# Kernel optimization log

Measured on AMD Instinct MI355X. Metric: run time of the kernel, lower is better.

The kernel has to match this reference:

```python
import jax, jax.numpy as jnp
import numpy as np

HEADS = 4

def _topk_mask(attn, k):
    # exact replica of mask.scatter_(-1, topk_indices, 1.0): exactly k ones per row
    C = attn.shape[-1]
    _, idx = jax.lax.top_k(attn, k)                      # [b,h,C,k]
    return jax.nn.one_hot(idx, C, dtype=attn.dtype).sum(axis=-2) > 0  # [b,h,C,C] bool


def setup_inputs() -> dict:
    key = jax.random.key(0)
    ks = jax.random.split(key, 8)
    b, dim, h, w = 32, 128, 4096, 1
    s = 0.05
    return {
        "x": jax.random.normal(ks[0], (b, dim, h, w), jnp.float32),
        "qkv_w": jax.random.normal(ks[1], (3 * dim, dim), jnp.float32) * s,
        "qkv_b": jax.random.normal(ks[2], (3 * dim,), jnp.float32) * s,
        "dw_w": jax.random.normal(ks[3], (3 * dim, 1, 3, 3), jnp.float32) * s,
        "dw_b": jax.random.normal(ks[4], (3 * dim,), jnp.float32) * s,
        "proj_w": jax.random.normal(ks[5], (dim, dim), jnp.float32) * s,
        "proj_b": jax.random.normal(ks[6], (dim,), jnp.float32) * s,
        "temperature": jnp.ones((HEADS, 1, 1), jnp.float32),
        "attn_w": jnp.full((4,), 0.2, jnp.float32),  # attn1..attn4
    }


def reference(x, qkv_w, qkv_b, dw_w, dw_b, proj_w, proj_b, temperature, attn_w):
    b, c, h, w = x.shape
    # 1x1 conv qkv, then 3x3 depthwise conv (groups = 3*c)
    qkv = jnp.einsum('bchw,oc->bohw', x, qkv_w) + qkv_b[None, :, None, None]
    qkv = jax.lax.conv_general_dilated(
        qkv, dw_w, window_strides=(1, 1), padding=((1, 1), (1, 1)),
        dimension_numbers=('NCHW', 'OIHW', 'NCHW'), feature_group_count=3 * c
    ) + dw_b[None, :, None, None]
    q, k, v = jnp.split(qkv, 3, axis=1)
    heads = lambda t: t.reshape(b, HEADS, c // HEADS, h * w)  # b head c (hw)
    q, k, v = heads(q), heads(k), heads(v)
    # F.normalize(dim=-1), eps=1e-12
    q = q / jnp.maximum(jnp.linalg.norm(q, axis=-1, keepdims=True), 1e-12)
    k = k / jnp.maximum(jnp.linalg.norm(k, axis=-1, keepdims=True), 1e-12)
    C = c // HEADS
    attn = jnp.einsum('bhcn,bhdn->bhcd', q, k) * temperature[None]  # [b,head,C,C]
    top_ks = [C // 2, (2 * C) // 3, (3 * C) // 4, (4 * C) // 5]
    out = jnp.zeros_like(v)
    for i, kk in enumerate(top_ks):
        m = _topk_mask(attn, kk)
        a = jax.nn.softmax(jnp.where(m, attn, -jnp.inf), axis=-1)
        out = out + attn_w[i] * jnp.einsum('bhcd,bhdn->bhcn', a, v)
    out = out.reshape(b, c, h, w)
    out = jnp.einsum('bchw,oc->bohw', out, proj_w) + proj_b[None, :, None, None]
    return out
```

## Files before the change

kernel.cpp:

```cpp
#include <hip/hip_runtime.h>

#define B_ 32
#define CD 128
#define O3 384
#define N  4096
#define H_ 4
#define C_ 32

typedef __bf16 bf16x8 __attribute__((ext_vector_type(8)));
typedef float floatx4 __attribute__((ext_vector_type(4)));

#define MFMA16(a, b, c) __builtin_amdgcn_mfma_f32_16x16x32_bf16(a, b, c, 0, 0, 0)

__device__ __forceinline__ float b2f(unsigned int u) {
  return __builtin_bit_cast(float, u << 16);
}
__device__ __forceinline__ float b2fh(unsigned int u) {
  return __builtin_bit_cast(float, u & 0xffff0000u);
}
__device__ __forceinline__ unsigned short f2b(float f) {
  unsigned int bits = __builtin_bit_cast(unsigned int, f);
  unsigned int r = (bits + 0x7FFFu + ((bits >> 16) & 1u)) >> 16;
  return (unsigned short)r;
}

__global__ __launch_bounds__(256) void k0_xt(const float* __restrict__ x,
                                             unsigned short* __restrict__ xT)
{
  __shared__ float xt[32 * 68];
  const int t = threadIdx.x;
  const int n0 = blockIdx.x * 64, c0 = blockIdx.y * 32, b = blockIdx.z;
  const float* xb = x + ((size_t)b * CD + c0) * N + n0;
#pragma unroll
  for (int i = 0; i < 2; i++) {
    int f = i * 256 + t;
    int c = f >> 4, n4 = (f & 15) * 4;
    float4 v = *(const float4*)(xb + (size_t)c * N + n4);
    *(float4*)&xt[c * 68 + n4] = v;
  }
  __syncthreads();
  int n = t >> 2, cb = (t & 3) * 8;
  unsigned short tmp[8];
#pragma unroll
  for (int j = 0; j < 8; j++) tmp[j] = f2b(xt[(cb + j) * 68 + n]);
  *(uint4*)(xT + ((size_t)b * N + n0 + n) * CD + c0 + cb) = *(uint4*)tmp;
}

__global__ void k0_w(const float* __restrict__ qkv_w,
                     const float* __restrict__ proj_w,
                     unsigned short* __restrict__ qkv_wb,
                     unsigned short* __restrict__ proj_wb)
{
  int e = (blockIdx.x * 256 + threadIdx.x) * 4;
  const float* src; unsigned short* dst; int off;
  if (e < 49152) { src = qkv_w; dst = qkv_wb; off = e; }
  else           { src = proj_w; dst = proj_wb; off = e - 49152; }
  float4 v = *(const float4*)(src + off);
  unsigned short tmp[4] = {f2b(v.x), f2b(v.y), f2b(v.z), f2b(v.w)};
  *(uint2*)(dst + off) = *(uint2*)tmp;
}

__global__ __launch_bounds__(256, 4) void k1_qkv_dw(
    const unsigned short* __restrict__ xT, const unsigned short* __restrict__ qkv_wb,
    const float* __restrict__ qkv_b, const float* __restrict__ dw_w,
    const float* __restrict__ dw_b, unsigned short* __restrict__ qkvd,
    unsigned short* __restrict__ vT)
{
  __shared__ __align__(16) char smem[34816];
  unsigned short* Bs   = (unsigned short*)smem;
  unsigned short* pres = (unsigned short*)smem;

  const int t = threadIdx.x;
  const int ytile = blockIdx.x, otile = blockIdx.y, b = blockIdx.z;
  const int obase = otile * 128;
  const int ybase = ytile * 124;
  const int wv = t >> 6, l = t & 63, quad = l >> 4, lm = l & 15;

#pragma unroll
  for (int i = 0; i < 8; i++) {
    int f = i * 256 + t;
    int row = f >> 4, c8 = (f & 15) * 8;
    int yg = ybase - 2 + row;
    uint4 v = make_uint4(0u, 0u, 0u, 0u);
    if (yg >= 0 && yg < N)
      v = *(const uint4*)(xT + ((size_t)b * N + yg) * CD + c8);
    *(uint4*)&Bs[row * 136 + c8] = v;
  }
  __syncthreads();

  floatx4 acc[2][8];
#pragma unroll
  for (int mt = 0; mt < 2; mt++)
#pragma unroll
    for (int nt = 0; nt < 8; nt++) acc[mt][nt] = (floatx4){0.f, 0.f, 0.f, 0.f};

  const unsigned short* wbase =
      qkv_wb + (size_t)(obase + wv * 32 + lm) * CD + quad * 8;
#pragma unroll
  for (int ks = 0; ks < 4; ks++) {
    bf16x8 a0 = *(const bf16x8*)(wbase + ks * 32);
    bf16x8 a1 = *(const bf16x8*)(wbase + 16 * CD + ks * 32);
#pragma unroll
    for (int nt = 0; nt < 8; nt++) {
      bf16x8 bb = *(const bf16x8*)&Bs[(nt * 16 + lm) * 136 + ks * 32 + quad * 8];
      acc[0][nt] = MFMA16(a0, bb, acc[0][nt]);
      acc[1][nt] = MFMA16(a1, bb, acc[1][nt]);
    }
  }

  if (otile < 2) {
    __syncthreads();
#pragma unroll
    for (int mt = 0; mt < 2; mt++)
#pragma unroll
      for (int r = 0; r < 4; r++) {
        int o = wv * 32 + mt * 16 + quad * 4 + r;
        float bias = qkv_b[obase + o];
#pragma unroll
        for (int nt = 0; nt < 8; nt++) {
          int i = nt * 16 + lm;
          if (i >= 1) {
            int yg = ybase - 2 + i;
            pres[o * 132 + (i - 1)] =
                f2b((yg >= 0 && yg < N) ? (acc[mt][nt][r] + bias) : 0.f);
          }
        }
      }
    __syncthreads();
    const int p = t & 63, og = t >> 6;
    const bool ok = (p < 62) && (ybase + 2 * p < N);
    const unsigned int* presu = (const unsigned int*)pres;
    for (int r2 = 0; r2 < 32; r2++) {
      int oo = __builtin_amdgcn_readfirstlane(obase + og * 32 + r2);
      float w0 = dw_w[oo * 9 + 1], w1 = dw_w[oo * 9 + 4],
            w2 = dw_w[oo * 9 + 7], db = dw_b[oo];
      int o = oo - obase;
      unsigned int u0 = presu[(o * 132 >> 1) + p];
      unsigned int u1 = presu[(o * 132 >> 1) + p + 1];
      float v0 = b2f(u0), v1 = b2fh(u0), v2 = b2f(u1), v3 = b2fh(u1);
      float out0 = w0 * v0 + w1 * v1 + w2 * v2 + db;
      float out1 = w0 * v1 + w1 * v2 + w2 * v3 + db;
      unsigned int pk = (unsigned int)f2b(out0) |
                        ((unsigned int)f2b(out1) << 16);
      if (ok)
        *(unsigned int*)(qkvd + ((size_t)b * 256 + oo) * N + ybase + 2 * p) = pk;
    }
  } else {
    const int o = t & 127, half = t >> 7;
    const int oo = obase + o;
    const float w0 = dw_w[oo * 9 + 1], w1 = dw_w[oo * 9 + 4],
                w2 = dw_w[oo * 9 + 7], db = dw_b[oo];
    __syncthreads();
#pragma unroll
    for (int mt = 0; mt < 2; mt++)
#pragma unroll
      for (int r = 0; r < 4; r++) {
        int o2 = wv * 32 + mt * 16 + quad * 4 + r;
        float bias = qkv_b[obase + o2];
#pragma unroll
        for (int nt = 0; nt < 8; nt++) {
          int i = nt * 16 + lm;
          int yg = ybase - 2 + i;
          pres[i * 132 + o2] =
              f2b((yg >= 0 && yg < N) ? (acc[mt][nt][r] + bias) : 0.f);
        }
      }
    __syncthreads();
    int i0 = 2 + half * 62;
    float pm = b2f((unsigned int)pres[(i0 - 1) * 132 + o]);
    float pc = b2f((unsigned int)pres[i0 * 132 + o]);
    for (int i = i0; i < i0 + 62; i++) {
      float pp = b2f((unsigned int)pres[(i + 1) * 132 + o]);
      int yo = ybase - 2 + i;
      if (yo < N) {
        float v = w0 * pm + w1 * pc + w2 * pp + db;
        vT[((size_t)b * N + yo) * CD + o] = f2b(v);
      }
      pm = pc; pc = pp;
    }
  }
}

__global__ __launch_bounds__(256, 4) void k3_gram(
    const unsigned short* __restrict__ qkvd, float* __restrict__ part)
{
  __shared__ float red[4 * 8 * 272];
  const int ns = blockIdx.x, h = blockIdx.y, b = blockIdx.z;
  const int t = threadIdx.x;
  const int wv = t >> 6, l = t & 63, quad = l >> 4, lm = l & 15;
  const unsigned short* qb = qkvd + ((size_t)b * 256 + h * C_) * N;
  const unsigned short* kb = qkvd + ((size_t)b * 256 + 128 + h * C_) * N;

  floatx4 acc[8];
#pragma unroll
  for (int i = 0; i < 8; i++) acc[i] = (floatx4){0.f, 0.f, 0.f, 0.f};

  const int nbase = ns * 1024 + wv * 32 + quad * 8;
#pragma unroll
  for (int ch = 0; ch < 8; ch++) {
    int nc = nbase + ch * 128;
    bf16x8 a0 = *(const bf16x8*)(qb + (size_t)lm * N + nc);
    bf16x8 a1 = *(const bf16x8*)(qb + (size_t)(16 + lm) * N + nc);
    bf16x8 b0 = *(const bf16x8*)(kb + (size_t)lm * N + nc);
    bf16x8 b1 = *(const bf16x8*)(kb + (size_t)(16 + lm) * N + nc);
    acc[0] = MFMA16(a0, b0, acc[0]);
    acc[1] = MFMA16(a0, b1, acc[1]);
    acc[2] = MFMA16(a1, b0, acc[2]);
    acc[3] = MFMA16(a1, b1, acc[3]);
    acc[4] = MFMA16(a0, a0, acc[4]);
    acc[5] = MFMA16(a1, a1, acc[5]);
    acc[6] = MFMA16(b0, b0, acc[6]);
    acc[7] = MFMA16(b1, b1, acc[7]);
  }

#pragma unroll
  for (int tl = 0; tl < 8; tl++)
#pragma unroll
    for (int r = 0; r < 4; r++)
      red[wv * 2176 + tl * 272 + (quad * 4 + r) * 17 + lm] = acc[tl][r];
  __syncthreads();

  float* pb = part + ((size_t)(b * H_ + h) * 4 + ns) * 2048;
  for (int e = t; e < 2048; e += 256) {
    int tl = e >> 8, rc = e & 255, row = rc >> 4, col = rc & 15;
    int a = tl * 272 + row * 17 + col;
    float s = red[a] + red[2176 + a] + red[2 * 2176 + a] + red[3 * 2176 + a];
    if (tl < 4) {
      int mt = tl >> 1, nt = tl & 1;
      pb[(mt * 16 + row) * 32 + nt * 16 + col] = s;
    } else if (row == col) {
      if (tl < 6) pb[1024 + (tl - 4) * 16 + row] = s;
      else        pb[1056 + (tl - 6) * 16 + row] = s;
    }
  }
}

__global__ __launch_bounds__(256) void k45(
    const float* __restrict__ part, const unsigned short* __restrict__ proj_wb,
    const float* __restrict__ temperature, const float* __restrict__ attn_w,
    unsigned short* __restrict__ Mb)
{
  __shared__ float La[H_][C_][33];
  __shared__ float sq2[256];
  __shared__ float rn[256];
  __shared__ float exL[H_][C_][33];
  __shared__ unsigned char rkL[H_][C_][C_];
  __shared__ unsigned short AwtT[H_][C_][40];
  const int b = blockIdx.x, t = threadIdx.x;

  const float* pbb = part + (size_t)b * 32768;
  for (int e = t; e < 4 * 2048; e += 256) {
    int h = e >> 11, idx = e & 2047;
    if (idx < 1088) {
      const float* p = pbb + h * 8192 + idx;
      float s = p[0] + p[2048] + p[2 * 2048] + p[3 * 2048];
      if (idx < 1024) La[h][idx >> 5][idx & 31] = s;
      else if (idx < 1056) sq2[h * 32 + (idx - 1024)] = s;
      else sq2[128 + h * 32 + (idx - 1056)] = s;
    }
  }
  __syncthreads();
  rn[t] = 1.f / fmaxf(sqrtf(sq2[t]), 1e-12f);
  __syncthreads();
  for (int e = t; e < 4096; e += 256) {
    int h = e >> 10, i = (e >> 5) & 31, j = e & 31;
    La[h][i][j] *= rn[h * 32 + i] * rn[128 + h * 32 + j] * temperature[h];
  }
  __syncthreads();

  if (t < 128) {
    int h = t >> 5, i = t & 31;
    float m = -1e30f;
    for (int j = 0; j < 32; j++) m = fmaxf(m, La[h][i][j]);
    float S0 = 0.f, S1 = 0.f, S2 = 0.f, S3 = 0.f;
    for (int j = 0; j < 32; j++) {
      float vj = La[h][i][j];
      int r = 0;
      for (int j2 = 0; j2 < 32; j2++) {
        float v2 = La[h][i][j2];
        r += (v2 > vj) || (v2 == vj && j2 < j);
      }
      float e = __expf(vj - m);
      exL[h][i][j] = e;
      rkL[h][i][j] = (unsigned char)r;
      if (r < 16) S0 += e;
      if (r < 21) S1 += e;
      if (r < 24) S2 += e;
      if (r < 25) S3 += e;
    }
    float w0 = attn_w[0] / S0, w1 = attn_w[1] / S1;
    float w2 = attn_w[2] / S2, w3 = attn_w[3] / S3;
    for (int j = 0; j < 32; j++) {
      int r = rkL[h][i][j];
      float cmb = (r < 16 ? w0 : 0.f) + (r < 21 ? w1 : 0.f) +
                  (r < 24 ? w2 : 0.f) + (r < 25 ? w3 : 0.f);
      AwtT[h][j][i] = f2b(exL[h][i][j] * cmb);
    }
  }
  __syncthreads();

  {
    const int wv = t >> 6, l = t & 63, quad = l >> 4, lm = l & 15;
    const int h = wv;
    bf16x8 bfr[2];
#pragma unroll
    for (int jt = 0; jt < 2; jt++)
      bfr[jt] = *(const bf16x8*)&AwtT[h][jt * 16 + lm][quad * 8];
#pragma unroll
    for (int mt = 0; mt < 8; mt++) {
      bf16x8 a = *(const bf16x8*)(proj_wb +
                    (size_t)(mt * 16 + lm) * CD + h * C_ + quad * 8);
#pragma unroll
      for (int jt = 0; jt < 2; jt++) {
        floatx4 acc = (floatx4){0.f, 0.f, 0.f, 0.f};
        acc = MFMA16(a, bfr[jt], acc);
#pragma unroll
        for (int r = 0; r < 4; r++) {
          int row = quad * 4 + r;
          Mb[(size_t)b * 16384 + (mt * 16 + row) * CD + h * C_ + jt * 16 + lm] =
              f2b(acc[r]);
        }
      }
    }
  }
}

__global__ __launch_bounds__(256, 4) void k6_out(
    const unsigned short* __restrict__ vT, const unsigned short* __restrict__ Mb,
    const float* __restrict__ proj_b, float* __restrict__ out)
{
  __shared__ unsigned short Bs[128 * 136];
  const int t = threadIdx.x;
  const int y0 = blockIdx.x * 128, b = blockIdx.y;
  const int wv = t >> 6, l = t & 63, quad = l >> 4, lm = l & 15;

#pragma unroll
  for (int i = 0; i < 8; i++) {
    int f = i * 256 + t;
    int row = f >> 4, c8 = (f & 15) * 8;
    *(uint4*)&Bs[row * 136 + c8] =
        *(const uint4*)(vT + ((size_t)b * N + y0 + row) * CD + c8);
  }
  __syncthreads();

  floatx4 acc[2][8];
#pragma unroll
  for (int mt = 0; mt < 2; mt++)
#pragma unroll
    for (int nt = 0; nt < 8; nt++) acc[mt][nt] = (floatx4){0.f, 0.f, 0.f, 0.f};

  const unsigned short* mbase =
      Mb + (size_t)b * 16384 + (size_t)(wv * 32 + lm) * CD + quad * 8;
#pragma unroll
  for (int ks = 0; ks < 4; ks++) {
    bf16x8 a0 = *(const bf16x8*)(mbase + ks * 32);
    bf16x8 a1 = *(const bf16x8*)(mbase + 16 * CD + ks * 32);
#pragma unroll
    for (int nt = 0; nt < 8; nt++) {
      bf16x8 bb = *(const bf16x8*)&Bs[(nt * 16 + lm) * 136 + ks * 32 + quad * 8];
      acc[0][nt] = MFMA16(a0, bb, acc[0][nt]);
      acc[1][nt] = MFMA16(a1, bb, acc[1][nt]);
    }
  }

#pragma unroll
  for (int mt = 0; mt < 2; mt++)
#pragma unroll
    for (int r = 0; r < 4; r++) {
      int o = wv * 32 + mt * 16 + quad * 4 + r;
      float pb = proj_b[o];
#pragma unroll
      for (int nt = 0; nt < 8; nt++) {
        int y = y0 + nt * 16 + lm;
        out[((size_t)b * CD + o) * N + y] = acc[mt][nt][r] + pb;
      }
    }
}

extern "C" void kernel_launch(void* const* d_in, const int* in_sizes, int n_in,
                              void* d_out, int out_size, void* d_ws, size_t ws_size,
                              hipStream_t stream)
{
  (void)in_sizes; (void)n_in; (void)out_size; (void)ws_size;
  const float* x           = (const float*)d_in[0];
  const float* qkv_w       = (const float*)d_in[1];
  const float* qkv_b       = (const float*)d_in[2];
  const float* dw_w        = (const float*)d_in[3];
  const float* dw_b        = (const float*)d_in[4];
  const float* proj_w      = (const float*)d_in[5];
  const float* proj_b      = (const float*)d_in[6];
  const float* temperature = (const float*)d_in[7];
  const float* attn_w      = (const float*)d_in[8];
  float* out = (float*)d_out;

  unsigned short* xT      = (unsigned short*)d_ws;
  unsigned short* qkv_wb  = xT + (size_t)16777216;
  unsigned short* proj_wb = qkv_wb + 49152;
  unsigned short* qkvd    = proj_wb + 16384;
  unsigned short* vT      = qkvd + (size_t)33554432;
  unsigned short* Mb      = vT + (size_t)16777216;
  float* part = (float*)(Mb + 524288);

  k0_xt    <<<dim3(64, 4, 32),  256, 0, stream>>>(x, xT);
  k0_w     <<<dim3(64),         256, 0, stream>>>(qkv_w, proj_w, qkv_wb, proj_wb);
  k1_qkv_dw<<<dim3(34, 3, 32),  256, 0, stream>>>(xT, qkv_wb, qkv_b, dw_w, dw_b,
                                                  qkvd, vT);
  k3_gram  <<<dim3(4, H_, B_),  256, 0, stream>>>(qkvd, part);
  k45      <<<dim3(B_),         256, 0, stream>>>(part, proj_wb, temperature,
                                                  attn_w, Mb);
  k6_out   <<<dim3(32, B_),     256, 0, stream>>>(vT, Mb, proj_b, out);
}
```

Measured before the change: 268.9 us.

## Fold depthwise conv taps into qkv weights and compute as single K=384 GEMM

Since w=1, the 3x3 depthwise conv reduces to a 3-tap conv along h, which is linear after the 1x1 qkv conv. The change folds the tap weights into a 384-wide weight matrix so each block runs one GEMM over three shifted copies of the input, with bias and boundary corrections precomputed. This removes the LDS staging pass and the separate depthwise loop, and the swizzled LDS layout is meant to avoid bank conflicts. In exchange it triples the MFMA work in k1 and rounds the tap-scaled weights to bf16. Workspace buffers Mb and part are reused for the new weights and bias tables before the kernels that later write to them.

```diff
diff --git a/kernel.cpp b/kernel.cpp
--- a/kernel.cpp
+++ b/kernel.cpp
@@ -48,135 +48,154 @@
 
 __global__ void k0_w(const float* __restrict__ qkv_w,
                      const float* __restrict__ proj_w,
-                     unsigned short* __restrict__ qkv_wb,
-                     unsigned short* __restrict__ proj_wb)
-{
-  int e = (blockIdx.x * 256 + threadIdx.x) * 4;
-  const float* src; unsigned short* dst; int off;
-  if (e < 49152) { src = qkv_w; dst = qkv_wb; off = e; }
-  else           { src = proj_w; dst = proj_wb; off = e - 49152; }
-  float4 v = *(const float4*)(src + off);
-  unsigned short tmp[4] = {f2b(v.x), f2b(v.y), f2b(v.z), f2b(v.w)};
-  *(uint2*)(dst + off) = *(uint2*)tmp;
+                     const float* __restrict__ dw_w,
+                     const float* __restrict__ dw_b,
+                     const float* __restrict__ qkv_b,
+                     unsigned short* __restrict__ qkv_wb2,
+                     unsigned short* __restrict__ proj_wb,
+                     float* __restrict__ sb,
+                     float* __restrict__ c0,
+                     float* __restrict__ c2)
+{
+  int e = blockIdx.x * 256 + threadIdx.x;
+  if (e < 36864) {
+    int base = e * 4;
+    int o = base / 384;
+    int k = base - o * 384;
+    int dlt = k >> 7, c = k & 127;
+    float w = dw_w[o * 9 + 1 + 3 * dlt];
+    float4 q = *(const float4*)(qkv_w + o * 128 + c);
+    unsigned short tmp[4] = {f2b(w * q.x), f2b(w * q.y), f2b(w * q.z),
+                             f2b(w * q.w)};
+    *(uint2*)(qkv_wb2 + base) = *(uint2*)tmp;
+  } else if (e < 40960) {
+    int base = (e - 36864) * 4;
+    float4 v = *(const float4*)(proj_w + base);
+    unsigned short tmp[4] = {f2b(v.x), f2b(v.y), f2b(v.z), f2b(v.w)};
+    *(uint2*)(proj_wb + base) = *(uint2*)tmp;
+  } else if (e < 41344) {
+    int o = e - 40960;
+    float w0 = dw_w[o * 9 + 1], w1 = dw_w[o * 9 + 4], w2 = dw_w[o * 9 + 7];
+    float qb = qkv_b[o], db = dw_b[o];
+    sb[o] = qb * (w0 + w1 + w2) + db;
+    c0[o] = qb * w0;
+    c2[o] = qb * w2;
+  }
 }
 
 __global__ __launch_bounds__(256, 4) void k1_qkv_dw(
-    const unsigned short* __restrict__ xT, const unsigned short* __restrict__ qkv_wb,
-    const float* __restrict__ qkv_b, const float* __restrict__ dw_w,
-    const float* __restrict__ dw_b, unsigned short* __restrict__ qkvd,
+    const unsigned short* __restrict__ xT,
+    const unsigned short* __restrict__ qkv_wb2,
+    const float* __restrict__ sb, const float* __restrict__ c0,
+    const float* __restrict__ c2, unsigned short* __restrict__ qkvd,
     unsigned short* __restrict__ vT)
 {
-  __shared__ __align__(16) char smem[34816];
-  unsigned short* Bs   = (unsigned short*)smem;
-  unsigned short* pres = (unsigned short*)smem;
-
+  __shared__ unsigned short Bs[128 * 128];
   const int t = threadIdx.x;
   const int ytile = blockIdx.x, otile = blockIdx.y, b = blockIdx.z;
   const int obase = otile * 128;
-  const int ybase = ytile * 124;
+  const int ybase = ytile * 126;
   const int wv = t >> 6, l = t & 63, quad = l >> 4, lm = l & 15;
 
 #pragma unroll
   for (int i = 0; i < 8; i++) {
     int f = i * 256 + t;
-    int row = f >> 4, c8 = (f & 15) * 8;
-    int yg = ybase - 2 + row;
+    int row = f >> 4, ch = f & 15;
+    int yg = ybase - 1 + row;
     uint4 v = make_uint4(0u, 0u, 0u, 0u);
     if (yg >= 0 && yg < N)
-      v = *(const uint4*)(xT + ((size_t)b * N + yg) * CD + c8);
-    *(uint4*)&Bs[row * 136 + c8] = v;
-  }
-  __syncthreads();
-
-  floatx4 acc[2][8];
-#pragma unroll
-  for (int mt = 0; mt < 2; mt++)
-#pragma unroll
-    for (int nt = 0; nt < 8; nt++) acc[mt][nt] = (floatx4){0.f, 0.f, 0.f, 0.f};
+      v = *(const uint4*)(xT + ((size_t)b * N + yg) * CD + ch * 8);
+    *(uint4*)&Bs[row * 128 + ((ch ^ (row & 15)) << 3)] = v;
+  }
+  __syncthreads();
 
   const unsigned short* wbase =
-      qkv_wb + (size_t)(obase + wv * 32 + lm) * CD + quad * 8;
-#pragma unroll
-  for (int ks = 0; ks < 4; ks++) {
-    bf16x8 a0 = *(const bf16x8*)(wbase + ks * 32);
-    bf16x8 a1 = *(const bf16x8*)(wbase + 16 * CD + ks * 32);
-#pragma unroll
-    for (int nt = 0; nt < 8; nt++) {
-      bf16x8 bb = *(const bf16x8*)&Bs[(nt * 16 + lm) * 136 + ks * 32 + quad * 8];
-      acc[0][nt] = MFMA16(a0, bb, acc[0][nt]);
-      acc[1][nt] = MFMA16(a1, bb, acc[1][nt]);
-    }
-  }
+      qkv_wb2 + (size_t)(obase + wv * 32 + lm) * 384 + quad * 8;
+  const bool edge = (ybase == 0) || (ybase + 126 >= N);
 
   if (otile < 2) {
-    __syncthreads();
+    floatx4 acc[2][8];
 #pragma unroll
     for (int mt = 0; mt < 2; mt++)
 #pragma unroll
+      for (int nt = 0; nt < 8; nt++) acc[mt][nt] = (floatx4){0.f, 0.f, 0.f, 0.f};
+
+#pragma unroll
+    for (int ks = 0; ks < 12; ks++) {
+      bf16x8 a0 = *(const bf16x8*)(wbase + ks * 32);
+      bf16x8 a1 = *(const bf16x8*)(wbase + 16 * 384 + ks * 32);
+      const int dlt = ks >> 2, cpart = ks & 3;
+      const int swz = (((cpart << 2) + quad) ^ ((lm + dlt) & 15)) << 3;
+#pragma unroll
+      for (int nt = 0; nt < 8; nt++) {
+        int rr = nt * 16 + lm + dlt;
+        if (nt == 7) rr = (rr > 127) ? 127 : rr;
+        bf16x8 bb = *(const bf16x8*)&Bs[rr * 128 + swz];
+        acc[0][nt] = MFMA16(a0, bb, acc[0][nt]);
+        acc[1][nt] = MFMA16(a1, bb, acc[1][nt]);
+      }
+    }
+
+#pragma unroll
+    for (int mt = 0; mt < 2; mt++)
+#pragma unroll
       for (int r = 0; r < 4; r++) {
-        int o = wv * 32 + mt * 16 + quad * 4 + r;
-        float bias = qkv_b[obase + o];
+        const int o = obase + wv * 32 + mt * 16 + quad * 4 + r;
+        const float bias = sb[o];
+        float c0v = 0.f, c2v = 0.f;
+        if (edge) { c0v = c0[o]; c2v = c2[o]; }
+        const size_t orow = ((size_t)b * 256 + o) * N;
 #pragma unroll
         for (int nt = 0; nt < 8; nt++) {
-          int i = nt * 16 + lm;
-          if (i >= 1) {
-            int yg = ybase - 2 + i;
-            pres[o * 132 + (i - 1)] =
-                f2b((yg >= 0 && yg < N) ? (acc[mt][nt][r] + bias) : 0.f);
-          }
+          int iy = nt * 16 + lm;
+          int y = ybase + iy;
+          float val = acc[mt][nt][r] + bias;
+          if (y == 0) val -= c0v;
+          if (y == N - 1) val -= c2v;
+          if (iy < 126 && y < N) qkvd[orow + y] = f2b(val);
         }
       }
-    __syncthreads();
-    const int p = t & 63, og = t >> 6;
-    const bool ok = (p < 62) && (ybase + 2 * p < N);
-    const unsigned int* presu = (const unsigned int*)pres;
-    for (int r2 = 0; r2 < 32; r2++) {
-      int oo = __builtin_amdgcn_readfirstlane(obase + og * 32 + r2);
-      float w0 = dw_w[oo * 9 + 1], w1 = dw_w[oo * 9 + 4],
-            w2 = dw_w[oo * 9 + 7], db = dw_b[oo];
-      int o = oo - obase;
-      unsigned int u0 = presu[(o * 132 >> 1) + p];
-      unsigned int u1 = presu[(o * 132 >> 1) + p + 1];
-      float v0 = b2f(u0), v1 = b2fh(u0), v2 = b2f(u1), v3 = b2fh(u1);
-      float out0 = w0 * v0 + w1 * v1 + w2 * v2 + db;
-      float out1 = w0 * v1 + w1 * v2 + w2 * v3 + db;
-      unsigned int pk = (unsigned int)f2b(out0) |
-                        ((unsigned int)f2b(out1) << 16);
-      if (ok)
-        *(unsigned int*)(qkvd + ((size_t)b * 256 + oo) * N + ybase + 2 * p) = pk;
-    }
   } else {
-    const int o = t & 127, half = t >> 7;
-    const int oo = obase + o;
-    const float w0 = dw_w[oo * 9 + 1], w1 = dw_w[oo * 9 + 4],
-                w2 = dw_w[oo * 9 + 7], db = dw_b[oo];
-    __syncthreads();
-#pragma unroll
-    for (int mt = 0; mt < 2; mt++)
-#pragma unroll
-      for (int r = 0; r < 4; r++) {
-        int o2 = wv * 32 + mt * 16 + quad * 4 + r;
-        float bias = qkv_b[obase + o2];
-#pragma unroll
-        for (int nt = 0; nt < 8; nt++) {
-          int i = nt * 16 + lm;
-          int yg = ybase - 2 + i;
-          pres[i * 132 + o2] =
-              f2b((yg >= 0 && yg < N) ? (acc[mt][nt][r] + bias) : 0.f);
+    floatx4 acc[8][2];
+#pragma unroll
+    for (int nt = 0; nt < 8; nt++)
+#pragma unroll
+      for (int mt = 0; mt < 2; mt++) acc[nt][mt] = (floatx4){0.f, 0.f, 0.f, 0.f};
+
+#pragma unroll
+    for (int ks = 0; ks < 12; ks++) {
+      bf16x8 a0 = *(const bf16x8*)(wbase + ks * 32);
+      bf16x8 a1 = *(const bf16x8*)(wbase + 16 * 384 + ks * 32);
+      const int dlt = ks >> 2, cpart = ks & 3;
+      const int swz = (((cpart << 2) + quad) ^ ((lm + dlt) & 15)) << 3;
+#pragma unroll
+      for (int nt = 0; nt < 8; nt++) {
+        int rr = nt * 16 + lm + dlt;
+        if (nt == 7) rr = (rr > 127) ? 127 : rr;
+        bf16x8 bb = *(const bf16x8*)&Bs[rr * 128 + swz];
+        acc[nt][0] = MFMA16(bb, a0, acc[nt][0]);
+        acc[nt][1] = MFMA16(bb, a1, acc[nt][1]);
+      }
+    }
+
+#pragma unroll
+    for (int mt = 0; mt < 2; mt++) {
+      const int ol = wv * 32 + mt * 16 + lm;
+      const float bias = sb[256 + ol];
+      float c0v = 0.f, c2v = 0.f;
+      if (edge) { c0v = c0[256 + ol]; c2v = c2[256 + ol]; }
+#pragma unroll
+      for (int nt = 0; nt < 8; nt++)
+#pragma unroll
+        for (int r = 0; r < 4; r++) {
+          int iy = nt * 16 + quad * 4 + r;
+          int y = ybase + iy;
+          float val = acc[nt][mt][r] + bias;
+          if (y == 0) val -= c0v;
+          if (y == N - 1) val -= c2v;
+          if (iy < 126 && y < N)
+            vT[((size_t)b * N + y) * CD + ol] = f2b(val);
         }
-      }
-    __syncthreads();
-    int i0 = 2 + half * 62;
-    float pm = b2f((unsigned int)pres[(i0 - 1) * 132 + o]);
-    float pc = b2f((unsigned int)pres[i0 * 132 + o]);
-    for (int i = i0; i < i0 + 62; i++) {
-      float pp = b2f((unsigned int)pres[(i + 1) * 132 + o]);
-      int yo = ybase - 2 + i;
-      if (yo < N) {
-        float v = w0 * pm + w1 * pc + w2 * pp + db;
-        vT[((size_t)b * N + yo) * CD + o] = f2b(v);
-      }
-      pm = pc; pc = pp;
     }
   }
 }
@@ -394,16 +413,21 @@
   float* out = (float*)d_out;
 
   unsigned short* xT      = (unsigned short*)d_ws;
-  unsigned short* qkv_wb  = xT + (size_t)16777216;
-  unsigned short* proj_wb = qkv_wb + 49152;
+  unsigned short* proj_wb = xT + (size_t)16777216;
   unsigned short* qkvd    = proj_wb + 16384;
   unsigned short* vT      = qkvd + (size_t)33554432;
   unsigned short* Mb      = vT + (size_t)16777216;
   float* part = (float*)(Mb + 524288);
+  unsigned short* qkv_wb2 = Mb;
+  float* sb = part;
+  float* c0 = part + 384;
+  float* c2 = part + 768;
 
   k0_xt    <<<dim3(64, 4, 32),  256, 0, stream>>>(x, xT);
-  k0_w     <<<dim3(64),         256, 0, stream>>>(qkv_w, proj_w, qkv_wb, proj_wb);
-  k1_qkv_dw<<<dim3(34, 3, 32),  256, 0, stream>>>(xT, qkv_wb, qkv_b, dw_w, dw_b,
+  k0_w     <<<dim3(162),        256, 0, stream>>>(qkv_w, proj_w, dw_w, dw_b,
+                                                  qkv_b, qkv_wb2, proj_wb,
+                                                  sb, c0, c2);
+  k1_qkv_dw<<<dim3(33, 3, 32),  256, 0, stream>>>(xT, qkv_wb2, sb, c0, c2,
                                                   qkvd, vT);
   k3_gram  <<<dim3(4, H_, B_),  256, 0, stream>>>(qkvd, part);
   k45      <<<dim3(B_),         256, 0, stream>>>(part, proj_wb, temperature,
```

Result: slower. 353.3 us (+31.4%).
